# Performance work log

Measured on AMD Instinct MI355X. Metric: run time of the kernel, lower is better.

Reference implementation:

```python
import jax, jax.numpy as jnp
import numpy as np

N = 100000
E = 1600000
D_IN = 128
D_HID = 128
D_OUT = 128


def setup_inputs() -> dict:
    key = jax.random.key(0)
    ks = jax.random.split(key, 12)
    x = jax.random.normal(ks[0], (N, D_IN), dtype=jnp.float32)
    edge_index = jax.random.randint(ks[1], (2, E), 0, N, dtype=jnp.int32)
    def lin(k, fan_in, fan_out):
        s = 1.0 / np.sqrt(fan_in)
        return jax.random.uniform(k, (fan_in, fan_out), jnp.float32, -s, s)
    dims = [(D_IN, D_HID), (D_HID, D_HID), (D_HID, D_OUT)]
    inp = {"x": x, "edge_index": edge_index}
    for i, (fi, fo) in enumerate(dims):
        inp[f"Wl{i}"] = lin(ks[2 + 3 * i], fi, fo)
        inp[f"Wr{i}"] = lin(ks[3 + 3 * i], fi, fo)
        inp[f"b{i}"] = jnp.zeros((fo,), jnp.float32)
    return inp


def _sage_conv(h, row, col, Wl, Wr, b):
    # mean aggregation over incoming neighbors: out[i] = mean_{j->i} h[j]
    n = h.shape[0]
    agg = jax.ops.segment_sum(h[col], row, num_segments=n)  # [N, d]
    deg = jax.ops.segment_sum(jnp.ones_like(row, dtype=h.dtype), row, num_segments=n)
    agg = agg / jnp.maximum(deg, 1.0)[:, None]
    return agg @ Wl + b + h @ Wr


def reference(x, edge_index, Wl0, Wr0, b0, Wl1, Wr1, b1, Wl2, Wr2, b2):
    row, col = edge_index[0], edge_index[1]  # dst, src
    h1 = jax.nn.relu(_sage_conv(x, row, col, Wl0, Wr0, b0))   # dropout is no-op in eval
    h2 = jax.nn.relu(_sage_conv(h1, row, col, Wl1, Wr1, b1))
    h3 = jax.nn.relu(_sage_conv(h2, row, col, Wl2, Wr2, b2))
    return (h1, h2, h3)
```

## Files before the change

### kernel.cpp

```cpp
#include <hip/hip_runtime.h>

#define NN 100000
#define NE 1600000
#define DD 128
#define BM 64
#define NPB 256
#define NBUCK 391
#define ECHUNK 8192
#define NBLK_PART 196
#define CAP 8192
#define CVX_BLK 800
#define CVW_BLK 384

typedef __attribute__((ext_vector_type(2))) float f32x2;
typedef __attribute__((ext_vector_type(4))) float f32x4;
typedef __attribute__((ext_vector_type(8))) short bf16x8;

__device__ inline unsigned short f2bf(float f) {
    unsigned int x = __builtin_bit_cast(unsigned int, f);
    unsigned int r = x + 0x7fffu + ((x >> 16) & 1u);
    return (unsigned short)(r >> 16);
}
__device__ inline unsigned int packbf(float a, float b) {
    return (unsigned int)f2bf(a) | ((unsigned int)f2bf(b) << 16);
}
__device__ inline unsigned int pk_fp8x4(float a, float b, float c, float d) {
    int v = 0;
    v = __builtin_amdgcn_cvt_pk_fp8_f32(a, b, v, false);
    v = __builtin_amdgcn_cvt_pk_fp8_f32(c, d, v, true);
    return (unsigned int)v;
}
__device__ inline f32x2 upk_fp8_lo(unsigned int v) {
    return __builtin_amdgcn_cvt_pk_f32_fp8((int)v, false);
}
__device__ inline f32x2 upk_fp8_hi(unsigned int v) {
    return __builtin_amdgcn_cvt_pk_f32_fp8((int)v, true);
}


__global__ __launch_bounds__(256) void prep_kernel(
    const float* __restrict__ x, unsigned short* __restrict__ xb,
    unsigned int* __restrict__ xf8,
    const float* __restrict__ w0, const float* __restrict__ w1,
    const float* __restrict__ w2, const float* __restrict__ w3,
    const float* __restrict__ w4, const float* __restrict__ w5,
    unsigned short* __restrict__ wtall,
    const int* __restrict__ row, int* __restrict__ gcnt) {
    __shared__ int cnt[NBUCK];
    const int b = blockIdx.x;
    if (b < CVX_BLK) {
        int i = b * 256 + threadIdx.x;
        const int n4 = NN * DD / 4;
        for (; i < n4; i += CVX_BLK * 256) {
            float4 v = reinterpret_cast<const float4*>(x)[i];
            ushort4 o;
            o.x = f2bf(v.x); o.y = f2bf(v.y); o.z = f2bf(v.z); o.w = f2bf(v.w);
            reinterpret_cast<ushort4*>(xb)[i] = o;
            xf8[i] = pk_fp8x4(v.x, v.y, v.z, v.w);
        }
    } else if (b < CVX_BLK + CVW_BLK) {
        int t = (b - CVX_BLK) * 256 + threadIdx.x;
        int i = t >> 14;
        int r = t & 16383;
        const float* W = (i == 0) ? w0 : (i == 1) ? w1 : (i == 2) ? w2
                        : (i == 3) ? w3 : (i == 4) ? w4 : w5;
        int c = r >> 7, k = r & 127;
        wtall[t] = f2bf(W[k * DD + c]);
    } else {
        for (int i = threadIdx.x; i < NBUCK; i += 256) cnt[i] = 0;
        __syncthreads();
        int base = (b - CVX_BLK - CVW_BLK) * ECHUNK;
        int end = base + ECHUNK; if (end > NE) end = NE;
        for (int i = base + threadIdx.x; i < end; i += 256)
            atomicAdd(&cnt[row[i] >> 8], 1);
        __syncthreads();
        for (int i = threadIdx.x; i < NBUCK; i += 256) {
            int c = cnt[i];
            if (c) atomicAdd(&gcnt[i], c);
        }
    }
}


__global__ __launch_bounds__(512) void bucket_scan(const int* __restrict__ gcnt,
                                                   int* __restrict__ gbase) {
    __shared__ int sm[512];
    int t = threadIdx.x;
    sm[t] = (t < NBUCK) ? gcnt[t] : 0;
    __syncthreads();
    for (int off = 1; off < 512; off <<= 1) {
        int add = (t >= off) ? sm[t - off] : 0;
        __syncthreads();
        sm[t] += add;
        __syncthreads();
    }
    if (t < NBUCK) gbase[t + 1] = sm[t];
    if (t == 0) gbase[0] = 0;
}

__global__ __launch_bounds__(256) void bucket_scatter(const int* __restrict__ row,
                                                      const int* __restrict__ col,
                                                      const int* __restrict__ gbase,
                                                      int* __restrict__ gcursor,
                                                      unsigned int* __restrict__ ebuf) {
    __shared__ int cnt[NBUCK];
    __shared__ int base[NBUCK];
    for (int i = threadIdx.x; i < NBUCK; i += 256) cnt[i] = 0;
    __syncthreads();
    int cbase = blockIdx.x * ECHUNK;
    int cend = cbase + ECHUNK; if (cend > NE) cend = NE;
    for (int i = cbase + threadIdx.x; i < cend; i += 256)
        atomicAdd(&cnt[row[i] >> 8], 1);
    __syncthreads();
    for (int i = threadIdx.x; i < NBUCK; i += 256) {
        int c = cnt[i];
        cnt[i] = 0;
        base[i] = c ? (gbase[i] + atomicAdd(&gcursor[i], c)) : 0;
    }
    __syncthreads();
    for (int i = cbase + threadIdx.x; i < cend; i += 256) {
        int r = row[i], c = col[i];
        int b = r >> 8;
        int k = atomicAdd(&cnt[b], 1);
        ebuf[base[b] + k] = ((unsigned)c << 8) | ((unsigned)r & 255u);
    }
}

__global__ __launch_bounds__(256) void csr_build(const unsigned int* __restrict__ ebuf,
                                                 const int* __restrict__ gbase,
                                                 int* __restrict__ offs,
                                                 int* __restrict__ csr_col) {
    __shared__ int dcnt[NPB];
    __shared__ int doff[NPB];
    __shared__ int sm[NPB];
    __shared__ int stage[CAP];
    const int b = blockIdx.x;
    const int es = gbase[b], ee = gbase[b + 1];
    const int m = ee - es;
    const int t = threadIdx.x;
    const int nbase = b * NPB;

    dcnt[t] = 0;
    __syncthreads();
    for (int i = es + t; i < ee; i += 256) {
        int ln = (int)(ebuf[i] & 255u);
        atomicAdd(&dcnt[ln], 1);
    }
    __syncthreads();
    sm[t] = dcnt[t];
    __syncthreads();
    for (int off = 1; off < 256; off <<= 1) {
        int add = (t >= off) ? sm[t - off] : 0;
        __syncthreads();
        sm[t] += add;
        __syncthreads();
    }
    doff[t] = sm[t] - dcnt[t];
    int node = nbase + t;
    if (node < NN) offs[node + 1] = es + sm[t];
    if (b == 0 && t == 0) offs[0] = 0;
    dcnt[t] = 0;
    __syncthreads();

    if (m <= CAP) {
        for (int i = es + t; i < ee; i += 256) {
            unsigned e = ebuf[i];
            int ln = (int)(e & 255u);
            int k = atomicAdd(&dcnt[ln], 1);
            stage[doff[ln] + k] = (int)(e >> 8);
        }
        __syncthreads();
        for (int i = t; i < m; i += 256) csr_col[es + i] = stage[i];
    } else {
        for (int i = es + t; i < ee; i += 256) {
            unsigned e = ebuf[i];
            int ln = (int)(e & 255u);
            int k = atomicAdd(&dcnt[ln], 1);
            csr_col[es + doff[ln] + k] = (int)(e >> 8);
        }
    }
}


__global__ __launch_bounds__(256) void fused_layer(
    const unsigned short* __restrict__ hb,
    const unsigned int* __restrict__ f8,
    const int* __restrict__ offs, const int* __restrict__ csr_col,
    const unsigned short* __restrict__ WlT, const unsigned short* __restrict__ WrT,
    const float* __restrict__ bias, float* __restrict__ out,
    unsigned short* __restrict__ hbn, unsigned int* __restrict__ f8n) {
    __shared__ uint4 smem4[1024];
    char* AldsB = (char*)smem4;
    const int row0 = blockIdx.x * BM;
    const int tid = threadIdx.x;
    const int w = tid >> 6, l = tid & 63;
    const int wr = w & 1, wc = w >> 1;
    const int lrow = l & 15, lg = l >> 4;

    bf16x8 aH[2][4];
#pragma unroll
    for (int m = 0; m < 2; ++m) {
        int gr = row0 + wr * 32 + m * 16 + lrow;
        if (gr >= NN) gr = NN - 1;
        const unsigned short* hrow = hb + (size_t)gr * DD;
#pragma unroll
        for (int kb = 0; kb < 4; ++kb)
            aH[m][kb] = *reinterpret_cast<const bf16x8*>(hrow + kb * 32 + lg * 8);
    }

    const int grp = tid >> 3, lane = tid & 7;
    const uint4* f84 = reinterpret_cast<const uint4*>(f8);
#pragma unroll
    for (int i = 0; i < 2; ++i) {
        const int rloc = grp * 2 + i;
        const int node = row0 + rloc;
        f32x2 a[8];
#pragma unroll
        for (int k = 0; k < 8; ++k) a[k] = (f32x2){0.f, 0.f};
        float inv = 0.0f;
        if (node < NN) {
            int s = offs[node], e = offs[node + 1];
            int p = s;
            for (; p + 8 <= e; p += 8) {
                uint4 v[8];
#pragma unroll
                for (int q = 0; q < 8; ++q)
                    v[q] = f84[(size_t)csr_col[p + q] * 8 + lane];
#pragma unroll
                for (int q = 0; q < 8; ++q) {
                    a[0] += upk_fp8_lo(v[q].x); a[1] += upk_fp8_hi(v[q].x);
                    a[2] += upk_fp8_lo(v[q].y); a[3] += upk_fp8_hi(v[q].y);
                    a[4] += upk_fp8_lo(v[q].z); a[5] += upk_fp8_hi(v[q].z);
                    a[6] += upk_fp8_lo(v[q].w); a[7] += upk_fp8_hi(v[q].w);
                }
            }
            for (; p < e; ++p) {
                uint4 v = f84[(size_t)csr_col[p] * 8 + lane];
                a[0] += upk_fp8_lo(v.x); a[1] += upk_fp8_hi(v.x);
                a[2] += upk_fp8_lo(v.y); a[3] += upk_fp8_hi(v.y);
                a[4] += upk_fp8_lo(v.z); a[5] += upk_fp8_hi(v.z);
                a[6] += upk_fp8_lo(v.w); a[7] += upk_fp8_hi(v.w);
            }
            inv = (e > s) ? (1.0f / (float)(e - s)) : 0.0f;
        }
        uint4 o0, o1;
        o0.x = packbf(a[0][0] * inv, a[0][1] * inv);
        o0.y = packbf(a[1][0] * inv, a[1][1] * inv);
        o0.z = packbf(a[2][0] * inv, a[2][1] * inv);
        o0.w = packbf(a[3][0] * inv, a[3][1] * inv);
        o1.x = packbf(a[4][0] * inv, a[4][1] * inv);
        o1.y = packbf(a[5][0] * inv, a[5][1] * inv);
        o1.z = packbf(a[6][0] * inv, a[6][1] * inv);
        o1.w = packbf(a[7][0] * inv, a[7][1] * inv);
        const int sw = (rloc & 7) << 4;
        const int rbase = rloc << 8;
        *reinterpret_cast<uint4*>(AldsB + rbase + ((lane * 32) ^ sw)) = o0;
        *reinterpret_cast<uint4*>(AldsB + rbase + ((lane * 32 + 16) ^ sw)) = o1;
    }
    __syncthreads();

    f32x4 acc[2][4];
#pragma unroll
    for (int m = 0; m < 2; ++m)
#pragma unroll
        for (int n = 0; n < 4; ++n) acc[m][n] = (f32x4){0.f, 0.f, 0.f, 0.f};

    float bv[4];
#pragma unroll
    for (int n = 0; n < 4; ++n) bv[n] = bias[wc * 64 + n * 16 + lrow];

#pragma unroll
    for (int kb = 0; kb < 4; ++kb) {
        const int kbyte = kb * 64 + lg * 16;
        bf16x8 aA[2];
#pragma unroll
        for (int m = 0; m < 2; ++m) {
            int rloc = wr * 32 + m * 16 + lrow;
            int off = (rloc << 8) + kbyte;
            off ^= (rloc & 7) << 4;
            aA[m] = *reinterpret_cast<const bf16x8*>(AldsB + off);
        }
        bf16x8 bL[4], bR[4];
#pragma unroll
        for (int n = 0; n < 4; ++n) {
            size_t woff = ((size_t)(wc * 64 + n * 16 + lrow) << 7) + kb * 32 + lg * 8;
            bL[n] = *reinterpret_cast<const bf16x8*>(WlT + woff);
            bR[n] = *reinterpret_cast<const bf16x8*>(WrT + woff);
        }
#pragma unroll
        for (int m = 0; m < 2; ++m)
#pragma unroll
            for (int n = 0; n < 4; ++n) {
                acc[m][n] = __builtin_amdgcn_mfma_f32_16x16x32_bf16(aA[m], bL[n], acc[m][n], 0, 0, 0);
                acc[m][n] = __builtin_amdgcn_mfma_f32_16x16x32_bf16(aH[m][kb], bR[n], acc[m][n], 0, 0, 0);
            }
    }

    __syncthreads();
    float* otile = (float*)smem4;
#pragma unroll
    for (int half = 0; half < 2; ++half) {
        if (wr == half) {
#pragma unroll
            for (int m = 0; m < 2; ++m) {
                int rb = m * 16 + lg * 4;
#pragma unroll
                for (int n = 0; n < 4; ++n) {
                    int c = wc * 64 + n * 16 + lrow;
#pragma unroll
                    for (int j = 0; j < 4; ++j)
                        otile[(rb + j) * DD + c] = fmaxf(acc[m][n][j] + bv[n], 0.0f);
                }
            }
        }
        __syncthreads();
        const f32x4* t4 = (const f32x4*)smem4;
#pragma unroll
        for (int it = 0; it < 4; ++it) {
            int idx = it * 256 + tid;
            int r = idx >> 5;
            int gr = row0 + half * 32 + r;
            if (gr < NN) {
                f32x4 v = t4[idx];
                __builtin_nontemporal_store(v, (f32x4*)out + (size_t)gr * 32 + (idx & 31));
                if (hbn) {
                    uint2 pk;
                    pk.x = packbf(v[0], v[1]);
                    pk.y = packbf(v[2], v[3]);
                    *((uint2*)hbn + (size_t)gr * 32 + (idx & 31)) = pk;
                    f8n[(size_t)gr * 32 + (idx & 31)] = pk_fp8x4(v[0], v[1], v[2], v[3]);
                }
            }
        }
        __syncthreads();
    }
}

extern "C" void kernel_launch(void* const* d_in, const int* in_sizes, int n_in,
                              void* d_out, int out_size, void* d_ws, size_t ws_size,
                              hipStream_t stream) {
    const float* x = (const float*)d_in[0];
    const int* ei = (const int*)d_in[1];
    const int* row = ei;
    const int* col = ei + NE;
    const float* Wl[3] = {(const float*)d_in[2], (const float*)d_in[5], (const float*)d_in[8]};
    const float* Wr[3] = {(const float*)d_in[3], (const float*)d_in[6], (const float*)d_in[9]};
    const float* bb[3] = {(const float*)d_in[4], (const float*)d_in[7], (const float*)d_in[10]};
    float* out = (float*)d_out;

    char* ws = (char*)d_ws;
    auto carve = [&](size_t bytes) {
        char* p = ws;
        ws += (bytes + 255) & ~(size_t)255;
        return p;
    };
    unsigned short* buf0 = (unsigned short*)carve((size_t)NN * DD * 2);
    unsigned short* buf1 = (unsigned short*)carve((size_t)NN * DD * 2);
    unsigned int* f8a = (unsigned int*)carve((size_t)NN * DD);
    unsigned int* f8b = (unsigned int*)carve((size_t)NN * DD);
    unsigned short* wtall = (unsigned short*)carve((size_t)6 * DD * DD * 2);
    int* gcnt    = (int*)carve((size_t)2 * NBUCK * sizeof(int));
    int* gcursor = gcnt + NBUCK;
    int* gbase   = (int*)carve((size_t)(NBUCK + 1) * sizeof(int));
    int* offs    = (int*)carve((size_t)(NN + 1) * sizeof(int));
    unsigned int* ebuf = (unsigned int*)carve((size_t)NE * sizeof(unsigned int));
    int* csr_col = (int*)carve((size_t)NE * sizeof(int));

    hipMemsetAsync(gcnt, 0, (size_t)2 * NBUCK * sizeof(int), stream);

    prep_kernel<<<CVX_BLK + CVW_BLK + NBLK_PART, 256, 0, stream>>>(
        x, buf0, f8a, Wl[0], Wr[0], Wl[1], Wr[1], Wl[2], Wr[2], wtall, row, gcnt);
    bucket_scan<<<1, 512, 0, stream>>>(gcnt, gbase);
    bucket_scatter<<<NBLK_PART, 256, 0, stream>>>(row, col, gbase, gcursor, ebuf);
    csr_build<<<NBUCK, 256, 0, stream>>>(ebuf, gbase, offs, csr_col);

    const int ngrid = (NN + BM - 1) / BM;

    unsigned short* hin = buf0;
    unsigned short* hout = buf1;
    unsigned int* f8in = f8a;
    unsigned int* f8out = f8b;
    for (int lyr = 0; lyr < 3; ++lyr) {
        float* o = out + (size_t)lyr * NN * DD;
        fused_layer<<<ngrid, 256, 0, stream>>>(
            hin, f8in, offs, csr_col,
            wtall + (size_t)2 * lyr * DD * DD, wtall + (size_t)(2 * lyr + 1) * DD * DD,
            bb[lyr], o,
            (lyr < 2) ? hout : (unsigned short*)nullptr,
            (lyr < 2) ? f8out : (unsigned int*)nullptr);
        unsigned short* t = hin; hin = hout; hout = t;
        unsigned int* t8 = f8in; f8in = f8out; f8out = t8;
    }
}
```

Measured before the change: 314.2 us.

## Drop bf16 activation copies; read fp32 self-features and convert in-kernel

Removes the separate bf16 copies of x and of each layer's output. Each layer now reads the fp32 self-features (x or the previous layer's output) with nontemporal loads and converts them to bf16 in registers, after the neighbour gather. The neighbour loop is also made branch-uniform by clamping indices and masking the tail in batches of 8. Other changes are launch_bounds occupancy 6 and fewer x-conversion blocks. This avoids writing and reading bf16 activation buffers at the cost of reading twice as many bytes for the self-feature rows.

```diff
diff --git a/kernel.cpp b/kernel.cpp
--- a/kernel.cpp
+++ b/kernel.cpp
@@ -9,7 +9,7 @@
 #define ECHUNK 8192
 #define NBLK_PART 196
 #define CAP 8192
-#define CVX_BLK 800
+#define CVX_BLK 512
 #define CVW_BLK 384
 
 typedef __attribute__((ext_vector_type(2))) float f32x2;
@@ -39,8 +39,7 @@
 
 
 __global__ __launch_bounds__(256) void prep_kernel(
-    const float* __restrict__ x, unsigned short* __restrict__ xb,
-    unsigned int* __restrict__ xf8,
+    const float* __restrict__ x, unsigned int* __restrict__ xf8,
     const float* __restrict__ w0, const float* __restrict__ w1,
     const float* __restrict__ w2, const float* __restrict__ w3,
     const float* __restrict__ w4, const float* __restrict__ w5,
@@ -53,9 +52,6 @@
         const int n4 = NN * DD / 4;
         for (; i < n4; i += CVX_BLK * 256) {
             float4 v = reinterpret_cast<const float4*>(x)[i];
-            ushort4 o;
-            o.x = f2bf(v.x); o.y = f2bf(v.y); o.z = f2bf(v.z); o.w = f2bf(v.w);
-            reinterpret_cast<ushort4*>(xb)[i] = o;
             xf8[i] = pk_fp8x4(v.x, v.y, v.z, v.w);
         }
     } else if (b < CVX_BLK + CVW_BLK) {
@@ -182,13 +178,13 @@
 }
 
 
-__global__ __launch_bounds__(256) void fused_layer(
-    const unsigned short* __restrict__ hb,
+__global__ __launch_bounds__(256, 6) void fused_layer(
+    const float* __restrict__ hsrc,
     const unsigned int* __restrict__ f8,
     const int* __restrict__ offs, const int* __restrict__ csr_col,
     const unsigned short* __restrict__ WlT, const unsigned short* __restrict__ WrT,
     const float* __restrict__ bias, float* __restrict__ out,
-    unsigned short* __restrict__ hbn, unsigned int* __restrict__ f8n) {
+    unsigned int* __restrict__ f8n) {
     __shared__ uint4 smem4[1024];
     char* AldsB = (char*)smem4;
     const int row0 = blockIdx.x * BM;
@@ -197,17 +193,6 @@
     const int wr = w & 1, wc = w >> 1;
     const int lrow = l & 15, lg = l >> 4;
 
-    bf16x8 aH[2][4];
-#pragma unroll
-    for (int m = 0; m < 2; ++m) {
-        int gr = row0 + wr * 32 + m * 16 + lrow;
-        if (gr >= NN) gr = NN - 1;
-        const unsigned short* hrow = hb + (size_t)gr * DD;
-#pragma unroll
-        for (int kb = 0; kb < 4; ++kb)
-            aH[m][kb] = *reinterpret_cast<const bf16x8*>(hrow + kb * 32 + lg * 8);
-    }
-
     const int grp = tid >> 3, lane = tid & 7;
     const uint4* f84 = reinterpret_cast<const uint4*>(f8);
 #pragma unroll
@@ -219,13 +204,19 @@
         for (int k = 0; k < 8; ++k) a[k] = (f32x2){0.f, 0.f};
         float inv = 0.0f;
         if (node < NN) {
-            int s = offs[node], e = offs[node + 1];
-            int p = s;
-            for (; p + 8 <= e; p += 8) {
+            const int s = offs[node], e = offs[node + 1];
+            const int emax = e - 1;
+            for (int p = s; p < e; p += 8) {
                 uint4 v[8];
 #pragma unroll
-                for (int q = 0; q < 8; ++q)
-                    v[q] = f84[(size_t)csr_col[p + q] * 8 + lane];
+                for (int q = 0; q < 8; ++q) {
+                    int idx = p + q;
+                    int ci = idx < emax ? idx : emax;
+                    int c = __builtin_nontemporal_load(csr_col + ci);
+                    v[q] = f84[(size_t)c * 8 + lane];
+                    unsigned msk = (idx < e) ? 0xFFFFFFFFu : 0u;
+                    v[q].x &= msk; v[q].y &= msk; v[q].z &= msk; v[q].w &= msk;
+                }
 #pragma unroll
                 for (int q = 0; q < 8; ++q) {
                     a[0] += upk_fp8_lo(v[q].x); a[1] += upk_fp8_hi(v[q].x);
@@ -233,13 +224,6 @@
                     a[4] += upk_fp8_lo(v[q].z); a[5] += upk_fp8_hi(v[q].z);
                     a[6] += upk_fp8_lo(v[q].w); a[7] += upk_fp8_hi(v[q].w);
                 }
-            }
-            for (; p < e; ++p) {
-                uint4 v = f84[(size_t)csr_col[p] * 8 + lane];
-                a[0] += upk_fp8_lo(v.x); a[1] += upk_fp8_hi(v.x);
-                a[2] += upk_fp8_lo(v.y); a[3] += upk_fp8_hi(v.y);
-                a[4] += upk_fp8_lo(v.z); a[5] += upk_fp8_hi(v.z);
-                a[6] += upk_fp8_lo(v.w); a[7] += upk_fp8_hi(v.w);
             }
             inv = (e > s) ? (1.0f / (float)(e - s)) : 0.0f;
         }
@@ -257,6 +241,27 @@
         *reinterpret_cast<uint4*>(AldsB + rbase + ((lane * 32) ^ sw)) = o0;
         *reinterpret_cast<uint4*>(AldsB + rbase + ((lane * 32 + 16) ^ sw)) = o1;
     }
+
+    bf16x8 aH[2][4];
+#pragma unroll
+    for (int m = 0; m < 2; ++m) {
+        int gr = row0 + wr * 32 + m * 16 + lrow;
+        if (gr >= NN) gr = NN - 1;
+        const float* hrow = hsrc + (size_t)gr * DD;
+#pragma unroll
+        for (int kb = 0; kb < 4; ++kb) {
+            f32x4 v0 = __builtin_nontemporal_load(
+                reinterpret_cast<const f32x4*>(hrow + kb * 32 + lg * 8));
+            f32x4 v1 = __builtin_nontemporal_load(
+                reinterpret_cast<const f32x4*>(hrow + kb * 32 + lg * 8 + 4));
+            uint4 pk;
+            pk.x = packbf(v0[0], v0[1]);
+            pk.y = packbf(v0[2], v0[3]);
+            pk.z = packbf(v1[0], v1[1]);
+            pk.w = packbf(v1[2], v1[3]);
+            aH[m][kb] = __builtin_bit_cast(bf16x8, pk);
+        }
+    }
     __syncthreads();
 
     f32x4 acc[2][4];
@@ -323,13 +328,8 @@
             if (gr < NN) {
                 f32x4 v = t4[idx];
                 __builtin_nontemporal_store(v, (f32x4*)out + (size_t)gr * 32 + (idx & 31));
-                if (hbn) {
-                    uint2 pk;
-                    pk.x = packbf(v[0], v[1]);
-                    pk.y = packbf(v[2], v[3]);
-                    *((uint2*)hbn + (size_t)gr * 32 + (idx & 31)) = pk;
+                if (f8n)
                     f8n[(size_t)gr * 32 + (idx & 31)] = pk_fp8x4(v[0], v[1], v[2], v[3]);
-                }
             }
         }
         __syncthreads();
@@ -354,8 +354,6 @@
         ws += (bytes + 255) & ~(size_t)255;
         return p;
     };
-    unsigned short* buf0 = (unsigned short*)carve((size_t)NN * DD * 2);
-    unsigned short* buf1 = (unsigned short*)carve((size_t)NN * DD * 2);
     unsigned int* f8a = (unsigned int*)carve((size_t)NN * DD);
     unsigned int* f8b = (unsigned int*)carve((size_t)NN * DD);
     unsigned short* wtall = (unsigned short*)carve((size_t)6 * DD * DD * 2);
@@ -369,26 +367,24 @@
     hipMemsetAsync(gcnt, 0, (size_t)2 * NBUCK * sizeof(int), stream);
 
     prep_kernel<<<CVX_BLK + CVW_BLK + NBLK_PART, 256, 0, stream>>>(
-        x, buf0, f8a, Wl[0], Wr[0], Wl[1], Wr[1], Wl[2], Wr[2], wtall, row, gcnt);
+        x, f8a, Wl[0], Wr[0], Wl[1], Wr[1], Wl[2], Wr[2], wtall, row, gcnt);
     bucket_scan<<<1, 512, 0, stream>>>(gcnt, gbase);
     bucket_scatter<<<NBLK_PART, 256, 0, stream>>>(row, col, gbase, gcursor, ebuf);
     csr_build<<<NBUCK, 256, 0, stream>>>(ebuf, gbase, offs, csr_col);
 
     const int ngrid = (NN + BM - 1) / BM;
 
-    unsigned short* hin = buf0;
-    unsigned short* hout = buf1;
+    const float* hsrc = x;
     unsigned int* f8in = f8a;
     unsigned int* f8out = f8b;
     for (int lyr = 0; lyr < 3; ++lyr) {
         float* o = out + (size_t)lyr * NN * DD;
         fused_layer<<<ngrid, 256, 0, stream>>>(
-            hin, f8in, offs, csr_col,
+            hsrc, f8in, offs, csr_col,
             wtall + (size_t)2 * lyr * DD * DD, wtall + (size_t)(2 * lyr + 1) * DD * DD,
             bb[lyr], o,
-            (lyr < 2) ? hout : (unsigned short*)nullptr,
             (lyr < 2) ? f8out : (unsigned int*)nullptr);
-        unsigned short* t = hin; hin = hout; hout = t;
+        hsrc = o;
         unsigned int* t8 = f8in; f8in = f8out; f8out = t8;
     }
 }
```

Result: slower. 503.7 us (+60.3%).
